# Kernel optimization log

Measured on AMD Instinct MI355X. Metric: run time of the kernel, lower is better.

Reference implementation:

```python
import jax, jax.numpy as jnp
import numpy as np

N, H, R, C = 50000, 16, 32, 8   # nodes, hidden, relations, classes
E = 1600000                      # edges (avg degree 32)


def setup_inputs() -> dict:
    key = jax.random.key(0)
    ks = jax.random.split(key, 6)
    edge_index = jax.random.randint(ks[0], (2, E), 0, N)
    edge_type = jax.random.randint(ks[1], (E,), 0, R)
    w1 = jax.random.normal(ks[2], (R, N, H), dtype=jnp.float32) * 0.05
    root1 = jax.random.normal(ks[3], (N, H), dtype=jnp.float32) * 0.05
    b1 = jnp.zeros((H,), jnp.float32)
    w2 = jax.random.normal(ks[4], (R, H, C), dtype=jnp.float32) * 0.05
    root2 = jax.random.normal(ks[5], (H, C), dtype=jnp.float32) * 0.05
    b2 = jnp.zeros((C,), jnp.float32)
    return {"edge_index": edge_index, "edge_type": edge_type,
            "w1": w1, "root1": root1, "b1": b1,
            "w2": w2, "root2": root2, "b2": b2}


def _rel_mean_agg(msgs, dst, edge_type, num_nodes, num_rel):
    """PyG RGCNConv aggregation: mean over edges within each (relation, target)
    pair, then sum over relations. msgs: [E, d] -> [num_nodes, d]."""
    seg = edge_type * num_nodes + dst                      # combined segment id
    tot = num_rel * num_nodes
    summed = jax.ops.segment_sum(msgs, seg, num_segments=tot)      # [R*N, d]
    cnt = jax.ops.segment_sum(jnp.ones((msgs.shape[0],), msgs.dtype), seg,
                              num_segments=tot)                    # [R*N]
    mean = summed / jnp.maximum(cnt, 1.0)[:, None]
    return mean.reshape(num_rel, num_nodes, -1).sum(axis=0)       # [N, d]


def reference(edge_index, edge_type, w1, root1, b1, w2, root2, b2):
    src, dst = edge_index[0], edge_index[1]
    # ---- layer 1: x = None -> message is weight row indexed by (rel, src)
    msgs1 = w1[edge_type, src]                             # [E, H] gather
    x = _rel_mean_agg(msgs1, dst, edge_type, N, R) + root1 + b1
    x = jax.nn.relu(x)
    # ---- layer 2: precompute per-relation transforms once: [R, N, C]
    xw = jnp.einsum('nh,rhc->rnc', x, w2)
    msgs2 = xw[edge_type, src]                             # [E, C] gather
    out = _rel_mean_agg(msgs2, dst, edge_type, N, R) + x @ root2 + b2
    return jax.nn.log_softmax(out, axis=1)
```

## Files before the change

### kernel.cpp

```cpp
#include <hip/hip_runtime.h>
#include <hip/hip_bf16.h>


constexpr int Nn = 50000;
constexpr int Hh = 16;
constexpr int Rr = 32;
constexpr int Cc = 8;
constexpr int Ee = 1600000;
constexpr int CHUNK = 4096;
constexpr int NC = (Ee + CHUNK - 1) / CHUNK;
constexpr int DSH = 7;
constexpr unsigned DLOWM = 127u;
constexpr int NBKT = (Nn + 127) / 128;

__device__ __forceinline__ float b2f(__hip_bfloat16 v) { return __bfloat162float(v); }

__global__ void sniff_kernel(const unsigned short* __restrict__ w, int* __restrict__ flag) {
    if (blockIdx.x == 0 && threadIdx.x == 0) {
        int hits = 0;
        for (int i = 0; i < 64; ++i) {
            unsigned short u = w[2 * i];
            int e = (u >> 7) & 0xFF;
            if (e >= 100 && e <= 130) ++hits;
        }
        *flag = (hits >= 32) ? 1 : 0;
    }
}

__global__ __launch_bounds__(256) void histA_kernel(const int* __restrict__ dst,
                                                    unsigned* __restrict__ H) {
    __shared__ unsigned hb[NBKT];
    int c = blockIdx.x, tid = threadIdx.x;
    for (int i = tid; i < NBKT; i += 256) hb[i] = 0;
    __syncthreads();
    int base = c * CHUNK;
    int n = min(CHUNK, Ee - base);
    for (int i = tid; i < n; i += 256)
        atomicAdd(&hb[((unsigned)dst[base + i]) >> DSH], 1u);
    __syncthreads();
    for (int i = tid; i < NBKT; i += 256) H[(size_t)c * NBKT + i] = hb[i];
}

__global__ __launch_bounds__(256) void scanB1_kernel(const unsigned* __restrict__ H,
                                                     unsigned* __restrict__ cb,
                                                     unsigned* __restrict__ bt) {
    __shared__ int lsum[4];
    int b = blockIdx.x, t = threadIdx.x, lane = t & 63, wv = t >> 6;
    int c0 = 2 * t, c1 = 2 * t + 1;
    int v0 = (c0 < NC) ? (int)H[(size_t)c0 * NBKT + b] : 0;
    int v1 = (c1 < NC) ? (int)H[(size_t)c1 * NBKT + b] : 0;
    int pair = v0 + v1, s = pair;
#pragma unroll
    for (int o = 1; o < 64; o <<= 1) { int u = __shfl_up(s, o, 64); if (lane >= o) s += u; }
    if (lane == 63) lsum[wv] = s;
    __syncthreads();
    int basev = 0;
    for (int j = 0; j < wv; ++j) basev += lsum[j];
    int incl = basev + s, eoff = incl - pair;
    if (c0 < NC) cb[(size_t)b * NC + c0] = (unsigned)eoff;
    if (c1 < NC) cb[(size_t)b * NC + c1] = (unsigned)(eoff + v0);
    if (t == 255) bt[b] = (unsigned)incl;
}

__global__ __launch_bounds__(256) void scanB2_kernel(const unsigned* __restrict__ bt,
                                                     unsigned* __restrict__ rbase) {
    __shared__ int lsum[4];
    int t = threadIdx.x, lane = t & 63, wv = t >> 6;
    int c0 = 2 * t, c1 = 2 * t + 1;
    int v0 = (c0 < NBKT) ? (int)bt[c0] : 0;
    int v1 = (c1 < NBKT) ? (int)bt[c1] : 0;
    int pair = v0 + v1, s = pair;
#pragma unroll
    for (int o = 1; o < 64; o <<= 1) { int u = __shfl_up(s, o, 64); if (lane >= o) s += u; }
    if (lane == 63) lsum[wv] = s;
    __syncthreads();
    int basev = 0;
    for (int j = 0; j < wv; ++j) basev += lsum[j];
    int incl = basev + s, eoff = incl - pair;
    if (c0 < NBKT) rbase[c0] = (unsigned)eoff;
    if (c1 < NBKT) rbase[c1] = (unsigned)(eoff + v0);
    if (t == 255) rbase[NBKT] = (unsigned)incl;
}

__global__ __launch_bounds__(256) void scatC_kernel(const int* __restrict__ src,
                                                    const int* __restrict__ dst,
                                                    const int* __restrict__ et,
                                                    const unsigned* __restrict__ cb,
                                                    const unsigned* __restrict__ rbase,
                                                    unsigned* __restrict__ rec) {
    __shared__ unsigned cbl[NBKT];
    __shared__ unsigned hb[NBKT];
    int c = blockIdx.x, tid = threadIdx.x;
    for (int i = tid; i < NBKT; i += 256) {
        cbl[i] = cb[(size_t)i * NC + c] + rbase[i];
        hb[i] = 0;
    }
    __syncthreads();
    int base = c * CHUNK;
    int n = min(CHUNK, Ee - base);
    for (int i = tid; i < n; i += 256) {
        int e = base + i;
        unsigned d = (unsigned)dst[e];
        unsigned r = (unsigned)et[e];
        unsigned sv = (unsigned)src[e];
        unsigned bkt = d >> DSH;
        unsigned rank = atomicAdd(&hb[bkt], 1u);
        unsigned pos = cbl[bkt] + rank;
        rec[pos] = sv | (r << 16) | ((d & DLOWM) << 21);
    }
}

__global__ __launch_bounds__(256) void sortD_kernel(const unsigned* __restrict__ rec,
                                                    const unsigned* __restrict__ rbase,
                                                    unsigned* __restrict__ sorted,
                                                    int* __restrict__ offs) {
    __shared__ unsigned cnt[128 * 33];
    __shared__ unsigned sbase[128 * 33];
    __shared__ int l2s[2];
    int b = blockIdx.x, t = threadIdx.x, lane = t & 63, wv = t >> 6;
    for (int i = t; i < 128 * 33; i += 256) { cnt[i] = 0; sbase[i] = 0; }
    __syncthreads();
    unsigned rb = rbase[b];
    unsigned re = (b == NBKT - 1) ? (unsigned)Ee : rbase[b + 1];
    int n = (int)(re - rb);
    for (int i = t; i < n; i += 256) {
        unsigned w = rec[rb + i];
        atomicAdd(&cnt[((w >> 21) & 127u) * 33 + ((w >> 16) & 31u)], 1u);
    }
    __syncthreads();
    int deg = 0;
    if (t < 128) {
#pragma unroll
        for (int r = 0; r < 32; ++r) {
            unsigned cc = cnt[t * 33 + r];
            sbase[t * 33 + r] = (unsigned)deg;
            deg += (int)cc;
        }
    }
    int s = deg;
#pragma unroll
    for (int o = 1; o < 64; o <<= 1) { int u = __shfl_up(s, o, 64); if (lane >= o) s += u; }
    if (lane == 63 && wv < 2) l2s[wv] = s;
    __syncthreads();
    if (t < 128) {
        int excl = s - deg + (wv == 1 ? l2s[0] : 0);
        unsigned ab = rb + (unsigned)excl;
        int d = b * 128 + t;
        if (d <= Nn) offs[d] = (int)ab;
#pragma unroll
        for (int r = 0; r < 32; ++r) sbase[t * 33 + r] += ab;
    }
    __syncthreads();
    for (int i = t; i < n; i += 256) {
        unsigned w = rec[rb + i];
        unsigned dlow = (w >> 21) & 127u, rel = (w >> 16) & 31u, sv = w & 0xFFFFu;
        int cell = (int)dlow * 33 + (int)rel;
        unsigned pos = atomicAdd(&sbase[cell], 1u);
        unsigned cc = cnt[cell];
        if (cc > 2047u) cc = 2047u;
        sorted[pos] = sv | (rel << 16) | (cc << 21);
    }
}

__global__ __launch_bounds__(256) void l1_kernel(const unsigned* __restrict__ sorted,
                                                 const int* __restrict__ offs,
                                                 const void* __restrict__ w1,
                                                 const void* __restrict__ root1,
                                                 const void* __restrict__ b1,
                                                 const int* __restrict__ flag,
                                                 float* __restrict__ x) {
    int tid = threadIdx.x, w = tid >> 6, lane = tid & 63;
    int ep = lane >> 3, hp = lane & 7;
    int isbf = *flag;
    int d = blockIdx.x * 4 + w;
    int off = offs[d], deg = offs[d + 1] - off;
    float a0 = 0.0f, a1 = 0.0f;
    if (isbf) {
#pragma unroll 2
        for (int i = ep; i < deg; i += 8) {
            unsigned p = sorted[off + i];
            int cnt = p >> 21, rel = (p >> 16) & 31, s = p & 0xFFFF;
            float inv = __builtin_amdgcn_rcpf((float)cnt);
            __hip_bfloat162 v = ((const __hip_bfloat162*)w1)[((size_t)rel * Nn + s) * 8 + hp];
            a0 += inv * __low2float(v); a1 += inv * __high2float(v);
        }
    } else {
#pragma unroll 2
        for (int i = ep; i < deg; i += 8) {
            unsigned p = sorted[off + i];
            int cnt = p >> 21, rel = (p >> 16) & 31, s = p & 0xFFFF;
            float inv = __builtin_amdgcn_rcpf((float)cnt);
            float2 v = ((const float2*)w1)[((size_t)rel * Nn + s) * 8 + hp];
            a0 += inv * v.x; a1 += inv * v.y;
        }
    }
#pragma unroll
    for (int o = 8; o < 64; o <<= 1) {
        a0 += __shfl_xor(a0, o, 64);
        a1 += __shfl_xor(a1, o, 64);
    }
    if (ep == 0) {
        float r0, r1v, bb0, bb1;
        if (isbf) {
            r0  = b2f(((const __hip_bfloat16*)root1)[d * Hh + hp * 2]);
            r1v = b2f(((const __hip_bfloat16*)root1)[d * Hh + hp * 2 + 1]);
            bb0 = b2f(((const __hip_bfloat16*)b1)[hp * 2]);
            bb1 = b2f(((const __hip_bfloat16*)b1)[hp * 2 + 1]);
        } else {
            r0  = ((const float*)root1)[d * Hh + hp * 2];
            r1v = ((const float*)root1)[d * Hh + hp * 2 + 1];
            bb0 = ((const float*)b1)[hp * 2];
            bb1 = ((const float*)b1)[hp * 2 + 1];
        }
        float v0 = a0 + r0 + bb0, v1 = a1 + r1v + bb1;
        *(float2*)(x + (size_t)d * Hh + hp * 2) =
            make_float2(v0 > 0.f ? v0 : 0.f, v1 > 0.f ? v1 : 0.f);
    }
}

__global__ __launch_bounds__(256) void l2_kernel(const unsigned* __restrict__ sorted,
                                                 const int* __restrict__ offs,
                                                 const float* __restrict__ x,
                                                 const void* __restrict__ w2,
                                                 const void* __restrict__ root2,
                                                 const void* __restrict__ b2v,
                                                 const int* __restrict__ flag,
                                                 void* __restrict__ out) {
    __shared__ float w2s[32 * 132];
    __shared__ float rsh[128];
    __shared__ float b2sh[8];
    int tid = threadIdx.x, w = tid >> 6, lane = tid & 63;
    int isbf = *flag;
    {
        int r = tid >> 3, cc = tid & 7;
        if (isbf) {
            const __hip_bfloat16* W = (const __hip_bfloat16*)w2 + r * 128 + cc;
#pragma unroll
            for (int h = 0; h < 16; ++h) w2s[r * 132 + cc * 16 + h] = b2f(W[h * 8]);
        } else {
            const float* W = (const float*)w2 + r * 128 + cc;
#pragma unroll
            for (int h = 0; h < 16; ++h) w2s[r * 132 + cc * 16 + h] = W[h * 8];
        }
    }
    if (tid < 128) rsh[tid] = isbf ? b2f(((const __hip_bfloat16*)root2)[tid])
                                   : ((const float*)root2)[tid];
    if (tid < 8)   b2sh[tid] = isbf ? b2f(((const __hip_bfloat16*)b2v)[tid])
                                    : ((const float*)b2v)[tid];
    __syncthreads();
    int ep = lane >> 3, c = lane & 7;
    int d = blockIdx.x * 4 + w;
    int off = offs[d], deg = offs[d + 1] - off;
    float acc = 0.0f;
    for (int i0 = 0; i0 < deg; i0 += 8) {
        int i = i0 + ep;
        if (i < deg) {
            unsigned p = sorted[off + i];
            int cnt = p >> 21, rel = (p >> 16) & 31, s = p & 0xFFFF;
            float inv = __builtin_amdgcn_rcpf((float)cnt);
            const float4* xr = (const float4*)(x + (size_t)s * Hh);
            float4 x0 = xr[0], x1 = xr[1], x2 = xr[2], x3 = xr[3];
            const float4* wv = (const float4*)(w2s + rel * 132 + c * 16);
            float4 w0 = wv[0], w1v = wv[1], w2v = wv[2], w3 = wv[3];
            float dot = x0.x*w0.x + x0.y*w0.y + x0.z*w0.z + x0.w*w0.w
                      + x1.x*w1v.x + x1.y*w1v.y + x1.z*w1v.z + x1.w*w1v.w
                      + x2.x*w2v.x + x2.y*w2v.y + x2.z*w2v.z + x2.w*w2v.w
                      + x3.x*w3.x + x3.y*w3.y + x3.z*w3.z + x3.w*w3.w;
            acc += inv * dot;
        }
    }
    acc += __shfl_xor(acc, 8, 64);
    acc += __shfl_xor(acc, 16, 64);
    acc += __shfl_xor(acc, 32, 64);
    if (ep == 0) {
        const float4* xr = (const float4*)(x + (size_t)d * Hh);
        float4 x0 = xr[0], x1 = xr[1], x2 = xr[2], x3 = xr[3];
        float xv[16] = {x0.x,x0.y,x0.z,x0.w, x1.x,x1.y,x1.z,x1.w,
                        x2.x,x2.y,x2.z,x2.w, x3.x,x3.y,x3.z,x3.w};
        float v = acc + b2sh[c];
#pragma unroll
        for (int h = 0; h < 16; ++h) v += xv[h] * rsh[h * 8 + c];
        float m = v;
#pragma unroll
        for (int o = 1; o < 8; o <<= 1) m = fmaxf(m, __shfl_xor(m, o, 8));
        float ssum = __expf(v - m);
#pragma unroll
        for (int o = 1; o < 8; o <<= 1) ssum += __shfl_xor(ssum, o, 8);
        float res = v - m - __logf(ssum);
        if (isbf) ((__hip_bfloat16*)out)[(size_t)d * Cc + c] = __float2bfloat16(res);
        else      ((float*)out)[(size_t)d * Cc + c] = res;
    }
}

extern "C" void kernel_launch(void* const* d_in, const int* in_sizes, int n_in,
                              void* d_out, int out_size, void* d_ws, size_t ws_size,
                              hipStream_t stream) {
    const int* edge_index = (const int*)d_in[0];
    const int* src = edge_index;
    const int* dst = edge_index + Ee;
    const int* et  = (const int*)d_in[1];
    const void* w1    = d_in[2];
    const void* root1 = d_in[3];
    const void* b1    = d_in[4];
    const void* w2    = d_in[5];
    const void* root2 = d_in[6];
    const void* b2    = d_in[7];

    unsigned* rec    = (unsigned*)d_ws;
    unsigned* sorted = rec + Ee;
    unsigned* H      = sorted + Ee;
    unsigned* cb     = H + (size_t)NC * NBKT;
    unsigned* bt     = cb + (size_t)NBKT * NC;
    unsigned* rbase  = bt + NBKT;
    int* offs        = (int*)(rbase + NBKT + 1);
    int* flag        = offs + Nn + 1;
    float* x         = (float*)rec;

    sniff_kernel<<<1, 64, 0, stream>>>((const unsigned short*)w1, flag);
    histA_kernel<<<NC, 256, 0, stream>>>(dst, H);
    scanB1_kernel<<<NBKT, 256, 0, stream>>>(H, cb, bt);
    scanB2_kernel<<<1, 256, 0, stream>>>(bt, rbase);
    scatC_kernel<<<NC, 256, 0, stream>>>(src, dst, et, cb, rbase, rec);
    sortD_kernel<<<NBKT, 256, 0, stream>>>(rec, rbase, sorted, offs);
    l1_kernel<<<Nn / 4, 256, 0, stream>>>(sorted, offs, w1, root1, b1, flag, x);
    l2_kernel<<<Nn / 4, 256, 0, stream>>>(sorted, offs, x, w2, root2, b2, flag, d_out);
}
```

Baseline: 306.7 us.

## Shrink sort chunks and buckets, scan in place, widen layer-1 gathers

Edge chunks drop from 4096 to 1024 and destination buckets from 128 to 64 nodes, so the bucket sort has more, lighter blocks and smaller shared histograms. The chunk-offset scan now runs in place on the histogram array with several chunks per thread, which removes the separate transposed offset buffer. The flag sniff kernel is folded into histA to save one launch. Layer 1 now gathers 16-byte vectors (4 hidden values per lane, 16 edges per wave step) instead of 8-byte pairs. The cost is a larger histogram matrix to scan and write, plus more blocks in the scatter and sort phases.

```diff
diff --git a/kernel.cpp b/kernel.cpp
--- a/kernel.cpp
+++ b/kernel.cpp
@@ -7,30 +7,34 @@
 constexpr int Rr = 32;
 constexpr int Cc = 8;
 constexpr int Ee = 1600000;
-constexpr int CHUNK = 4096;
+constexpr int CHUNK = 1024;
 constexpr int NC = (Ee + CHUNK - 1) / CHUNK;
-constexpr int DSH = 7;
-constexpr unsigned DLOWM = 127u;
-constexpr int NBKT = (Nn + 127) / 128;
+constexpr int DSH = 6;
+constexpr unsigned DLOWM = 63u;
+constexpr int NBKT = (Nn + 63) / 64;
+constexpr int K1 = (NC + 255) / 256;
+constexpr int K2 = (NBKT + 255) / 256;
 
 __device__ __forceinline__ float b2f(__hip_bfloat16 v) { return __bfloat162float(v); }
-
-__global__ void sniff_kernel(const unsigned short* __restrict__ w, int* __restrict__ flag) {
-    if (blockIdx.x == 0 && threadIdx.x == 0) {
+__device__ __forceinline__ float bs2f(unsigned short u) {
+    return __uint_as_float(((unsigned)u) << 16);
+}
+
+__global__ __launch_bounds__(256) void histA_kernel(const int* __restrict__ dst,
+                                                    unsigned* __restrict__ H,
+                                                    const unsigned short* __restrict__ w1s,
+                                                    int* __restrict__ flag) {
+    __shared__ unsigned hb[NBKT];
+    int c = blockIdx.x, tid = threadIdx.x;
+    if (c == 0 && tid == 0) {
         int hits = 0;
         for (int i = 0; i < 64; ++i) {
-            unsigned short u = w[2 * i];
+            unsigned short u = w1s[2 * i];
             int e = (u >> 7) & 0xFF;
             if (e >= 100 && e <= 130) ++hits;
         }
         *flag = (hits >= 32) ? 1 : 0;
     }
-}
-
-__global__ __launch_bounds__(256) void histA_kernel(const int* __restrict__ dst,
-                                                    unsigned* __restrict__ H) {
-    __shared__ unsigned hb[NBKT];
-    int c = blockIdx.x, tid = threadIdx.x;
     for (int i = tid; i < NBKT; i += 256) hb[i] = 0;
     __syncthreads();
     int base = c * CHUNK;
@@ -41,58 +45,77 @@
     for (int i = tid; i < NBKT; i += 256) H[(size_t)c * NBKT + i] = hb[i];
 }
 
-__global__ __launch_bounds__(256) void scanB1_kernel(const unsigned* __restrict__ H,
-                                                     unsigned* __restrict__ cb,
+__global__ __launch_bounds__(256) void scanB1_kernel(unsigned* __restrict__ H,
                                                      unsigned* __restrict__ bt) {
     __shared__ int lsum[4];
     int b = blockIdx.x, t = threadIdx.x, lane = t & 63, wv = t >> 6;
-    int c0 = 2 * t, c1 = 2 * t + 1;
-    int v0 = (c0 < NC) ? (int)H[(size_t)c0 * NBKT + b] : 0;
-    int v1 = (c1 < NC) ? (int)H[(size_t)c1 * NBKT + b] : 0;
-    int pair = v0 + v1, s = pair;
+    int c0 = t * K1;
+    int v[K1];
+#pragma unroll
+    for (int j = 0; j < K1; ++j) {
+        int c = c0 + j;
+        v[j] = (c < NC) ? (int)H[(size_t)c * NBKT + b] : 0;
+    }
+    int tot = 0;
+#pragma unroll
+    for (int j = 0; j < K1; ++j) { int tmp = v[j]; v[j] = tot; tot += tmp; }
+    int s = tot;
 #pragma unroll
     for (int o = 1; o < 64; o <<= 1) { int u = __shfl_up(s, o, 64); if (lane >= o) s += u; }
     if (lane == 63) lsum[wv] = s;
     __syncthreads();
     int basev = 0;
     for (int j = 0; j < wv; ++j) basev += lsum[j];
-    int incl = basev + s, eoff = incl - pair;
-    if (c0 < NC) cb[(size_t)b * NC + c0] = (unsigned)eoff;
-    if (c1 < NC) cb[(size_t)b * NC + c1] = (unsigned)(eoff + v0);
-    if (t == 255) bt[b] = (unsigned)incl;
+    int excl = basev + s - tot;
+#pragma unroll
+    for (int j = 0; j < K1; ++j) {
+        int c = c0 + j;
+        if (c < NC) H[(size_t)c * NBKT + b] = (unsigned)(excl + v[j]);
+    }
+    if (t == 255) bt[b] = (unsigned)(basev + s);
 }
 
 __global__ __launch_bounds__(256) void scanB2_kernel(const unsigned* __restrict__ bt,
                                                      unsigned* __restrict__ rbase) {
     __shared__ int lsum[4];
     int t = threadIdx.x, lane = t & 63, wv = t >> 6;
-    int c0 = 2 * t, c1 = 2 * t + 1;
-    int v0 = (c0 < NBKT) ? (int)bt[c0] : 0;
-    int v1 = (c1 < NBKT) ? (int)bt[c1] : 0;
-    int pair = v0 + v1, s = pair;
+    int c0 = t * K2;
+    int v[K2];
+#pragma unroll
+    for (int j = 0; j < K2; ++j) {
+        int c = c0 + j;
+        v[j] = (c < NBKT) ? (int)bt[c] : 0;
+    }
+    int tot = 0;
+#pragma unroll
+    for (int j = 0; j < K2; ++j) { int tmp = v[j]; v[j] = tot; tot += tmp; }
+    int s = tot;
 #pragma unroll
     for (int o = 1; o < 64; o <<= 1) { int u = __shfl_up(s, o, 64); if (lane >= o) s += u; }
     if (lane == 63) lsum[wv] = s;
     __syncthreads();
     int basev = 0;
     for (int j = 0; j < wv; ++j) basev += lsum[j];
-    int incl = basev + s, eoff = incl - pair;
-    if (c0 < NBKT) rbase[c0] = (unsigned)eoff;
-    if (c1 < NBKT) rbase[c1] = (unsigned)(eoff + v0);
-    if (t == 255) rbase[NBKT] = (unsigned)incl;
+    int excl = basev + s - tot;
+#pragma unroll
+    for (int j = 0; j < K2; ++j) {
+        int c = c0 + j;
+        if (c < NBKT) rbase[c] = (unsigned)(excl + v[j]);
+    }
+    if (t == 255) rbase[NBKT] = (unsigned)(basev + s);
 }
 
 __global__ __launch_bounds__(256) void scatC_kernel(const int* __restrict__ src,
                                                     const int* __restrict__ dst,
                                                     const int* __restrict__ et,
-                                                    const unsigned* __restrict__ cb,
+                                                    const unsigned* __restrict__ H,
                                                     const unsigned* __restrict__ rbase,
                                                     unsigned* __restrict__ rec) {
-    __shared__ unsigned cbl[NBKT];
+    __shared__ unsigned bb[NBKT];
     __shared__ unsigned hb[NBKT];
     int c = blockIdx.x, tid = threadIdx.x;
     for (int i = tid; i < NBKT; i += 256) {
-        cbl[i] = cb[(size_t)i * NC + c] + rbase[i];
+        bb[i] = H[(size_t)c * NBKT + i] + rbase[i];
         hb[i] = 0;
     }
     __syncthreads();
@@ -105,8 +128,7 @@
         unsigned sv = (unsigned)src[e];
         unsigned bkt = d >> DSH;
         unsigned rank = atomicAdd(&hb[bkt], 1u);
-        unsigned pos = cbl[bkt] + rank;
-        rec[pos] = sv | (r << 16) | ((d & DLOWM) << 21);
+        rec[bb[bkt] + rank] = sv | (r << 16) | ((d & DLOWM) << 21);
     }
 }
 
@@ -114,48 +136,41 @@
                                                     const unsigned* __restrict__ rbase,
                                                     unsigned* __restrict__ sorted,
                                                     int* __restrict__ offs) {
-    __shared__ unsigned cnt[128 * 33];
-    __shared__ unsigned sbase[128 * 33];
-    __shared__ int l2s[2];
-    int b = blockIdx.x, t = threadIdx.x, lane = t & 63, wv = t >> 6;
-    for (int i = t; i < 128 * 33; i += 256) { cnt[i] = 0; sbase[i] = 0; }
-    __syncthreads();
-    unsigned rb = rbase[b];
-    unsigned re = (b == NBKT - 1) ? (unsigned)Ee : rbase[b + 1];
+    __shared__ unsigned cnt[64 * 33];
+    __shared__ unsigned sb[64 * 33];
+    int b = blockIdx.x, t = threadIdx.x;
+    for (int i = t; i < 64 * 33; i += 256) cnt[i] = 0;
+    __syncthreads();
+    unsigned rb = rbase[b], re = rbase[b + 1];
     int n = (int)(re - rb);
     for (int i = t; i < n; i += 256) {
         unsigned w = rec[rb + i];
-        atomicAdd(&cnt[((w >> 21) & 127u) * 33 + ((w >> 16) & 31u)], 1u);
-    }
-    __syncthreads();
-    int deg = 0;
-    if (t < 128) {
+        atomicAdd(&cnt[((w >> 21) & 63u) * 33 + ((w >> 16) & 31u)], 1u);
+    }
+    __syncthreads();
+    if (t < 64) {
+        int deg = 0;
 #pragma unroll
         for (int r = 0; r < 32; ++r) {
             unsigned cc = cnt[t * 33 + r];
-            sbase[t * 33 + r] = (unsigned)deg;
+            sb[t * 33 + r] = (unsigned)deg;
             deg += (int)cc;
         }
-    }
-    int s = deg;
-#pragma unroll
-    for (int o = 1; o < 64; o <<= 1) { int u = __shfl_up(s, o, 64); if (lane >= o) s += u; }
-    if (lane == 63 && wv < 2) l2s[wv] = s;
-    __syncthreads();
-    if (t < 128) {
-        int excl = s - deg + (wv == 1 ? l2s[0] : 0);
-        unsigned ab = rb + (unsigned)excl;
-        int d = b * 128 + t;
+        int s = deg;
+#pragma unroll
+        for (int o = 1; o < 64; o <<= 1) { int u = __shfl_up(s, o, 64); if (t >= o) s += u; }
+        unsigned ab = rb + (unsigned)(s - deg);
+        int d = b * 64 + t;
         if (d <= Nn) offs[d] = (int)ab;
 #pragma unroll
-        for (int r = 0; r < 32; ++r) sbase[t * 33 + r] += ab;
+        for (int r = 0; r < 32; ++r) sb[t * 33 + r] += ab;
     }
     __syncthreads();
     for (int i = t; i < n; i += 256) {
         unsigned w = rec[rb + i];
-        unsigned dlow = (w >> 21) & 127u, rel = (w >> 16) & 31u, sv = w & 0xFFFFu;
+        unsigned dlow = (w >> 21) & 63u, rel = (w >> 16) & 31u, sv = w & 0xFFFFu;
         int cell = (int)dlow * 33 + (int)rel;
-        unsigned pos = atomicAdd(&sbase[cell], 1u);
+        unsigned pos = atomicAdd(&sb[cell], 1u);
         unsigned cc = cnt[cell];
         if (cc > 2047u) cc = 2047u;
         sorted[pos] = sv | (rel << 16) | (cc << 21);
@@ -170,51 +185,56 @@
                                                  const int* __restrict__ flag,
                                                  float* __restrict__ x) {
     int tid = threadIdx.x, w = tid >> 6, lane = tid & 63;
-    int ep = lane >> 3, hp = lane & 7;
+    int ep = lane >> 2, hp = lane & 3;
     int isbf = *flag;
     int d = blockIdx.x * 4 + w;
     int off = offs[d], deg = offs[d + 1] - off;
-    float a0 = 0.0f, a1 = 0.0f;
+    float a0 = 0.f, a1 = 0.f, a2 = 0.f, a3 = 0.f;
     if (isbf) {
 #pragma unroll 2
-        for (int i = ep; i < deg; i += 8) {
+        for (int i = ep; i < deg; i += 16) {
             unsigned p = sorted[off + i];
             int cnt = p >> 21, rel = (p >> 16) & 31, s = p & 0xFFFF;
             float inv = __builtin_amdgcn_rcpf((float)cnt);
-            __hip_bfloat162 v = ((const __hip_bfloat162*)w1)[((size_t)rel * Nn + s) * 8 + hp];
-            a0 += inv * __low2float(v); a1 += inv * __high2float(v);
+            ushort4 v = ((const ushort4*)w1)[((size_t)rel * Nn + s) * 4 + hp];
+            a0 += inv * bs2f(v.x); a1 += inv * bs2f(v.y);
+            a2 += inv * bs2f(v.z); a3 += inv * bs2f(v.w);
         }
     } else {
 #pragma unroll 2
-        for (int i = ep; i < deg; i += 8) {
+        for (int i = ep; i < deg; i += 16) {
             unsigned p = sorted[off + i];
             int cnt = p >> 21, rel = (p >> 16) & 31, s = p & 0xFFFF;
             float inv = __builtin_amdgcn_rcpf((float)cnt);
-            float2 v = ((const float2*)w1)[((size_t)rel * Nn + s) * 8 + hp];
-            a0 += inv * v.x; a1 += inv * v.y;
-        }
-    }
-#pragma unroll
-    for (int o = 8; o < 64; o <<= 1) {
+            float4 v = ((const float4*)w1)[((size_t)rel * Nn + s) * 4 + hp];
+            a0 += inv * v.x; a1 += inv * v.y; a2 += inv * v.z; a3 += inv * v.w;
+        }
+    }
+#pragma unroll
+    for (int o = 4; o < 64; o <<= 1) {
         a0 += __shfl_xor(a0, o, 64);
         a1 += __shfl_xor(a1, o, 64);
+        a2 += __shfl_xor(a2, o, 64);
+        a3 += __shfl_xor(a3, o, 64);
     }
     if (ep == 0) {
-        float r0, r1v, bb0, bb1;
+        float r0, r1, r2, r3, bb0, bb1, bb2, bb3;
         if (isbf) {
-            r0  = b2f(((const __hip_bfloat16*)root1)[d * Hh + hp * 2]);
-            r1v = b2f(((const __hip_bfloat16*)root1)[d * Hh + hp * 2 + 1]);
-            bb0 = b2f(((const __hip_bfloat16*)b1)[hp * 2]);
-            bb1 = b2f(((const __hip_bfloat16*)b1)[hp * 2 + 1]);
+            ushort4 rv = ((const ushort4*)root1)[(size_t)d * 4 + hp];
+            ushort4 bv = ((const ushort4*)b1)[hp];
+            r0 = bs2f(rv.x); r1 = bs2f(rv.y); r2 = bs2f(rv.z); r3 = bs2f(rv.w);
+            bb0 = bs2f(bv.x); bb1 = bs2f(bv.y); bb2 = bs2f(bv.z); bb3 = bs2f(bv.w);
         } else {
-            r0  = ((const float*)root1)[d * Hh + hp * 2];
-            r1v = ((const float*)root1)[d * Hh + hp * 2 + 1];
-            bb0 = ((const float*)b1)[hp * 2];
-            bb1 = ((const float*)b1)[hp * 2 + 1];
-        }
-        float v0 = a0 + r0 + bb0, v1 = a1 + r1v + bb1;
-        *(float2*)(x + (size_t)d * Hh + hp * 2) =
-            make_float2(v0 > 0.f ? v0 : 0.f, v1 > 0.f ? v1 : 0.f);
+            float4 rv = ((const float4*)root1)[(size_t)d * 4 + hp];
+            float4 bv = ((const float4*)b1)[hp];
+            r0 = rv.x; r1 = rv.y; r2 = rv.z; r3 = rv.w;
+            bb0 = bv.x; bb1 = bv.y; bb2 = bv.z; bb3 = bv.w;
+        }
+        float v0 = a0 + r0 + bb0, v1 = a1 + r1 + bb1;
+        float v2 = a2 + r2 + bb2, v3 = a3 + r3 + bb3;
+        *(float4*)(x + (size_t)d * Hh + hp * 4) =
+            make_float4(v0 > 0.f ? v0 : 0.f, v1 > 0.f ? v1 : 0.f,
+                        v2 > 0.f ? v2 : 0.f, v3 > 0.f ? v3 : 0.f);
     }
 }
 
@@ -309,18 +329,16 @@
     unsigned* rec    = (unsigned*)d_ws;
     unsigned* sorted = rec + Ee;
     unsigned* H      = sorted + Ee;
-    unsigned* cb     = H + (size_t)NC * NBKT;
-    unsigned* bt     = cb + (size_t)NBKT * NC;
+    unsigned* bt     = H + (size_t)NC * NBKT;
     unsigned* rbase  = bt + NBKT;
     int* offs        = (int*)(rbase + NBKT + 1);
-    int* flag        = offs + Nn + 1;
+    int* flag        = offs + Nn + 4;
     float* x         = (float*)rec;
 
-    sniff_kernel<<<1, 64, 0, stream>>>((const unsigned short*)w1, flag);
-    histA_kernel<<<NC, 256, 0, stream>>>(dst, H);
-    scanB1_kernel<<<NBKT, 256, 0, stream>>>(H, cb, bt);
+    histA_kernel<<<NC, 256, 0, stream>>>(dst, H, (const unsigned short*)w1, flag);
+    scanB1_kernel<<<NBKT, 256, 0, stream>>>(H, bt);
     scanB2_kernel<<<1, 256, 0, stream>>>(bt, rbase);
-    scatC_kernel<<<NC, 256, 0, stream>>>(src, dst, et, cb, rbase, rec);
+    scatC_kernel<<<NC, 256, 0, stream>>>(src, dst, et, H, rbase, rec);
     sortD_kernel<<<NBKT, 256, 0, stream>>>(rec, rbase, sorted, offs);
     l1_kernel<<<Nn / 4, 256, 0, stream>>>(sorted, offs, w1, root1, b1, flag, x);
     l2_kernel<<<Nn / 4, 256, 0, stream>>>(sorted, offs, x, w2, root2, b2, flag, d_out);
```

Result: no change. 312.4 us (+1.8%).
